# Kernel tuning notes

Measured on AMD Instinct MI355X. Metric: run time of the kernel, lower is better.

Reference implementation:

```python
import jax, jax.numpy as jnp
import numpy as np

NP, P = 5, 5  # number of body parts, joints per part


def _windows(t):
    # (binf, length) for the 6 overlapping temporal windows of sequence()
    h, th = t // 2, t // 3
    return [(0, t), (0, h), (h, t - h), (0, th), (th, th), (2 * th, t - 2 * th)]


def _block(xw):
    # xw: (B, NP, P, L, C) -> Gaussian-embedding blocks (B, NP, L, C+1, C+1)
    B, n, p, L, C = xw.shape
    # smoothing over the P (joint-within-part) axis, as in the original code
    xs = xw.at[:, :, 1:-1].set((xw[:, :, 1:-1] + xw[:, :, :-2] + xw[:, :, 2:]) / 3)
    mu = xs.mean(axis=2)  # (B, NP, L, C)
    # temporally shifted centered slices (shifts over the L axis)
    x0 = xw - mu[:, :, None]                       # (B, NP, P, L, C)
    xm = xw[:, :, :, :-2] - mu[:, :, None, 1:-1]   # (B, NP, P, L-2, C)
    xp = xw[:, :, :, 2:] - mu[:, :, None, 1:-1]    # (B, NP, P, L-2, C)
    outer_mean = lambda a: jnp.einsum('bnptc,bnptd->bntcd', a, a) / p
    cov_mid = (outer_mean(xm) + outer_mean(x0[:, :, :, 1:-1]) + outer_mean(xp)) / 3
    xb = x0[:, :, :, ::L - 1]  # boundary frames 0 and L-1
    cov_b = jnp.einsum('bnptc,bnptd->bntcd', xb, xb) / p
    cov = jnp.zeros((B, n, L, C, C), xw.dtype)
    cov = cov.at[:, :, 1:-1].set(cov_mid)
    cov = cov.at[:, :, ::L - 1].set(cov_b)
    elt00 = cov + mu[..., :, None] * mu[..., None, :]  # cov + mu mu^T
    top = jnp.concatenate([elt00, mu[..., None]], axis=-1)            # (.., C, C+1)
    ones = jnp.ones((B, n, L, 1, 1), xw.dtype)
    bot = jnp.concatenate([mu[..., None, :], ones], axis=-1)          # (.., 1, C+1)
    return jnp.concatenate([top, bot], axis=-2)                        # (.., C+1, C+1)


def setup_inputs() -> dict:
    key = jax.random.key(0)
    x = jax.random.normal(key, (256, 600, 25, 3, 1), dtype=jnp.float32)
    return {"input": x}


def reference(input):
    B, T, J, C, _ = input.shape
    # (B, T, J, C, 1) -> (B, NP, P, T, C)  (matches transpose(1,2).reshape)
    x = jnp.moveaxis(input[..., 0], 1, 2).reshape(B, NP, P, T, C)
    blocks = [_block(x[:, :, :, b:b + L]) for b, L in _windows(T)]
    return jnp.concatenate(blocks, axis=2)  # (B, NP, sum(L_s), C+1, C+1)
```

## Files before the change

kernel.cpp:

```cpp
#include <hip/hip_runtime.h>


#define T_ 600
#define CH_ 100
#define NCH_ 6

__global__ __launch_bounds__(256) void gauss_agg_kernel(const float* __restrict__ x,
                                                        float* __restrict__ out) {
    __shared__ float raw[102 * 75];
    __shared__ float4 obuf[256 * 5];

    int blk = blockIdx.x;
    int ch  = blk % NCH_;
    int b   = blk / NCH_;

    int start = ch * CH_ - 1; if (start < 0) start = 0;
    int end   = ch * CH_ + CH_ + 1; if (end > T_) end = T_;
    int total = (end - start) * 75;

    const float* src = x + ((size_t)b * T_ + start) * 75;
    for (int e = (int)threadIdx.x; e < total; e += 256) raw[e] = src[e];
    __syncthreads();

    int ofs = (ch == 0) ? 0 : 1;
    const float w5[5] = {4.f, 2.f, 3.f, 2.f, 4.f};
    float4* outf4 = reinterpret_cast<float4*>(out);

    for (int m = 0; m < 6; ++m) {
        int s = m * 256 + (int)threadIdx.x;
        if (s < 1500) {
            int n  = s / 300;
            int q  = s - n * 300;
            int w  = q / 100;
            int tl = q - w * 100;
            int tt = ch * CH_ + tl;
            int li = tl + ofs;

            bool boundary;
            if (w == 0)      boundary = (tt == 0) || (tt == 599);
            else if (w == 1) boundary = (tt == 0) || (tt == 299) || (tt == 300) || (tt == 599);
            else             boundary = (tt == 0) || (tt == 199) || (tt == 200) ||
                                        (tt == 399) || (tt == 400) || (tt == 599);

            const float* rc = &raw[li * 75 + n * 15];

            float s0=0.f,s1=0.f,s2=0.f, m0=0.f,m1=0.f,m2=0.f;
            float A00=0.f,A01=0.f,A02=0.f,A11=0.f,A12=0.f,A22=0.f;
            #pragma unroll
            for (int p = 0; p < 5; ++p) {
                float a = rc[p*3+0], c = rc[p*3+1], d = rc[p*3+2];
                s0 += a; s1 += c; s2 += d;
                m0 += w5[p]*a; m1 += w5[p]*c; m2 += w5[p]*d;
                A00 += a*a; A01 += a*c; A02 += a*d;
                A11 += c*c; A12 += c*d; A22 += d*d;
            }
            float mu0 = m0*(1.f/15.f), mu1 = m1*(1.f/15.f), mu2 = m2*(1.f/15.f);

            float inv = 0.2f;
            if (!boundary) {
                #pragma unroll
                for (int dstep = 0; dstep < 2; ++dstep) {
                    const float* rn = rc + (dstep ? 75 : -75);
                    #pragma unroll
                    for (int p = 0; p < 5; ++p) {
                        float a = rn[p*3+0], c = rn[p*3+1], d = rn[p*3+2];
                        s0 += a; s1 += c; s2 += d;
                        A00 += a*a; A01 += a*c; A02 += a*d;
                        A11 += c*c; A12 += c*d; A22 += d*d;
                    }
                }
                inv = 1.f/15.f;
            }

            float mb0 = s0*inv, mb1 = s1*inv, mb2 = s2*inv;
            float e00 = A00*inv - 2.f*mu0*mb0 + 2.f*mu0*mu0;
            float e01 = A01*inv - mu0*mb1 - mb0*mu1 + 2.f*mu0*mu1;
            float e02 = A02*inv - mu0*mb2 - mb0*mu2 + 2.f*mu0*mu2;
            float e11 = A11*inv - 2.f*mu1*mb1 + 2.f*mu1*mu1;
            float e12 = A12*inv - mu1*mb2 - mb1*mu2 + 2.f*mu1*mu2;
            float e22 = A22*inv - 2.f*mu2*mb2 + 2.f*mu2*mu2;

            int base = (int)threadIdx.x * 5;
            obuf[base + 0] = make_float4(e00, e01, e02, mu0);
            obuf[base + 1] = make_float4(e01, e11, e12, mu1);
            obuf[base + 2] = make_float4(e02, e12, e22, mu2);
            obuf[base + 3] = make_float4(mu0, mu1, mu2, 1.f);
        }
        __syncthreads();

        int nslots  = (1500 - m * 256 < 256) ? (1500 - m * 256) : 256;
        int npieces = nslots * 4;
        #pragma unroll
        for (int k = 0; k < 4; ++k) {
            int f = k * 256 + (int)threadIdx.x;
            if (f < npieces) {
                int sl = f >> 2, pc = f & 3;
                int s2 = m * 256 + sl;
                int n  = s2 / 300;
                int q  = s2 - n * 300;
                int w  = q / 100;
                int tl = q - w * 100;
                int tt = ch * CH_ + tl;
                size_t o = ((size_t)(b * 5 + n) * 1800 + w * 600 + tt) * 4 + pc;
                outf4[o] = obuf[sl * 5 + pc];
            }
        }
        __syncthreads();
    }
}

extern "C" void kernel_launch(void* const* d_in, const int* in_sizes, int n_in,
                              void* d_out, int out_size, void* d_ws, size_t ws_size,
                              hipStream_t stream) {
    const float* x = (const float*)d_in[0];
    float* out = (float*)d_out;
    gauss_agg_kernel<<<256 * NCH_, 256, 0, stream>>>(x, out);
}
```

Baseline: 42.13 us.

## Repartition blocks by (batch, part, window-group, half) for contiguous output writes

```diff
diff --git a/kernel.cpp b/kernel.cpp
--- a/kernel.cpp
+++ b/kernel.cpp
@@ -2,47 +2,54 @@
 
 
 #define T_ 600
-#define CH_ 100
-#define NCH_ 6
 
 __global__ __launch_bounds__(256) void gauss_agg_kernel(const float* __restrict__ x,
                                                         float* __restrict__ out) {
-    __shared__ float raw[102 * 75];
+    __shared__ float raw[301 * 15];
     __shared__ float4 obuf[256 * 5];
 
     int blk = blockIdx.x;
-    int ch  = blk % NCH_;
-    int b   = blk / NCH_;
+    int oct = blk & 7;
+    int inner = blk >> 3;
+    int bh = inner / 30;
+    int r  = inner - bh * 30;
+    int n = r / 6;
+    int r2 = r - n * 6;
+    int g = r2 >> 1;
+    int half = r2 & 1;
+    int b = oct + 8 * bh;
+    int tt0 = half * 300;
 
-    int start = ch * CH_ - 1; if (start < 0) start = 0;
-    int end   = ch * CH_ + CH_ + 1; if (end > T_) end = T_;
-    int total = (end - start) * 75;
+    int start = tt0 - 1; if (start < 0) start = 0;
+    int end   = tt0 + 301; if (end > T_) end = T_;
+    int nrows = end - start;
+    int ofs   = tt0 - start;
 
-    const float* src = x + ((size_t)b * T_ + start) * 75;
-    for (int e = (int)threadIdx.x; e < total; e += 256) raw[e] = src[e];
+    const float* src = x + ((size_t)b * T_ + start) * 75 + n * 15;
+    int tot = nrows * 15;
+    for (int e = (int)threadIdx.x; e < tot; e += 256) {
+        int row = e / 15;
+        int c   = e - row * 15;
+        raw[e] = src[row * 75 + c];
+    }
     __syncthreads();
 
-    int ofs = (ch == 0) ? 0 : 1;
     const float w5[5] = {4.f, 2.f, 3.f, 2.f, 4.f};
     float4* outf4 = reinterpret_cast<float4*>(out);
+    size_t obase = ((size_t)(b * 5 + n) * 1800 + g * 600 + tt0) * 4;
 
-    for (int m = 0; m < 6; ++m) {
-        int s = m * 256 + (int)threadIdx.x;
-        if (s < 1500) {
-            int n  = s / 300;
-            int q  = s - n * 300;
-            int w  = q / 100;
-            int tl = q - w * 100;
-            int tt = ch * CH_ + tl;
+    for (int m = 0; m < 2; ++m) {
+        int tl = m * 256 + (int)threadIdx.x;
+        if (tl < 300) {
+            int tt = tt0 + tl;
             int li = tl + ofs;
 
             bool boundary;
-            if (w == 0)      boundary = (tt == 0) || (tt == 599);
-            else if (w == 1) boundary = (tt == 0) || (tt == 299) || (tt == 300) || (tt == 599);
-            else             boundary = (tt == 0) || (tt == 199) || (tt == 200) ||
-                                        (tt == 399) || (tt == 400) || (tt == 599);
+            if (g == 0)      boundary = (tt == 0) || (tt == 599);
+            else if (g == 1) { int q = tt % 300; boundary = (q == 0) || (q == 299); }
+            else             { int q = tt % 200; boundary = (q == 0) || (q == 199); }
 
-            const float* rc = &raw[li * 75 + n * 15];
+            const float* rc = &raw[li * 15];
 
             float s0=0.f,s1=0.f,s2=0.f, m0=0.f,m1=0.f,m2=0.f;
             float A00=0.f,A01=0.f,A02=0.f,A11=0.f,A12=0.f,A22=0.f;
@@ -60,7 +67,7 @@
             if (!boundary) {
                 #pragma unroll
                 for (int dstep = 0; dstep < 2; ++dstep) {
-                    const float* rn = rc + (dstep ? 75 : -75);
+                    const float* rn = rc + (dstep ? 15 : -15);
                     #pragma unroll
                     for (int p = 0; p < 5; ++p) {
                         float a = rn[p*3+0], c = rn[p*3+1], d = rn[p*3+2];
@@ -88,21 +95,14 @@
         }
         __syncthreads();
 
-        int nslots  = (1500 - m * 256 < 256) ? (1500 - m * 256) : 256;
+        int nslots = 300 - m * 256; if (nslots > 256) nslots = 256;
         int npieces = nslots * 4;
         #pragma unroll
         for (int k = 0; k < 4; ++k) {
             int f = k * 256 + (int)threadIdx.x;
             if (f < npieces) {
                 int sl = f >> 2, pc = f & 3;
-                int s2 = m * 256 + sl;
-                int n  = s2 / 300;
-                int q  = s2 - n * 300;
-                int w  = q / 100;
-                int tl = q - w * 100;
-                int tt = ch * CH_ + tl;
-                size_t o = ((size_t)(b * 5 + n) * 1800 + w * 600 + tt) * 4 + pc;
-                outf4[o] = obuf[sl * 5 + pc];
+                outf4[obase + (size_t)(m * 256 + sl) * 4 + pc] = obuf[sl * 5 + pc];
             }
         }
         __syncthreads();
@@ -114,5 +114,5 @@
                               hipStream_t stream) {
     const float* x = (const float*)d_in[0];
     float* out = (float*)d_out;
-    gauss_agg_kernel<<<256 * NCH_, 256, 0, stream>>>(x, out);
+    gauss_agg_kernel<<<256 * 30, 256, 0, stream>>>(x, out);
 }
```

Result: slower. 47.98 us (+13.9%).
